# Kernel tuning notes

Hardware: AMD Instinct MI355X
Metric: run time of the kernel (lower is better)

## Reference

```python
import jax, jax.numpy as jnp
import numpy as np

B, L, C = 16, 2048, 256
H, R = 6, 32
HEAD_SCALE = 1.0 / np.sqrt(R)


def setup_inputs() -> dict:
    key = jax.random.key(0)
    k1, k2, k3, k4 = jax.random.split(key, 4)
    feats = jax.random.normal(k1, (B, L + 1, C), dtype=jnp.float32)
    Wq = jax.random.normal(k2, (H * R, C), dtype=jnp.float32) * (1.0 / np.sqrt(C))
    Wk = jax.random.normal(k3, (H * R, C), dtype=jnp.float32) * (1.0 / np.sqrt(C))
    Wd = jax.random.normal(k4, (1, C), dtype=jnp.float32) * (1.0 / np.sqrt(C))
    bd = jnp.zeros((1,), dtype=jnp.float32)
    logit_scale = jnp.ones((), dtype=jnp.float32)
    return {"feats": feats, "Wq": Wq, "Wk": Wk, "Wd": Wd, "bd": bd,
            "logit_scale": logit_scale}


def _fold_vertices(feats):
    # drop leading token, pair-average: [B, L+1, C] -> [B, L//2, C]
    x = feats[:, 1:]
    b, l, c = x.shape
    return x.reshape(b, l // 2, 2, c).mean(axis=2)


def reference(feats, Wq, Wk, Wd, bd, logit_scale):
    x = _fold_vertices(feats)                     # [B, N, C]
    b, n, _ = x.shape
    Q = (x @ Wq.T).reshape(b, n, H, R)            # [B, N, H, R]
    K = (x @ Wk.T).reshape(b, n, H, R)
    # sum over heads of per-head low-rank QK^T == contraction over folded (H*R)
    S = jnp.einsum('bnhr,bmhr->bnm', Q, K) * HEAD_SCALE   # [B, N, N]
    d = (x @ Wd.T + bd).squeeze(-1)               # [B, N]
    idx = jnp.arange(n)
    S = S.at[:, idx, idx].add(d)
    return S * jnp.maximum(logit_scale, 0.01)
```

## Files before the change

kernel.cpp:

```cpp
#include <hip/hip_runtime.h>
#include <stdint.h>


#define HD_SCALE 0.17677669529663687f

typedef __bf16 bf16_t;
typedef bf16_t bf16x8 __attribute__((ext_vector_type(8)));
typedef float f32x4 __attribute__((ext_vector_type(4)));

__device__ __forceinline__ unsigned short f2bf(float f) {
  unsigned int u = __float_as_uint(f);
  return (unsigned short)((u + 0x7fffu + ((u >> 16) & 1u)) >> 16);
}

__device__ __forceinline__ void gload16(const void* g, void* l) {
  __builtin_amdgcn_global_load_lds(
      (const __attribute__((address_space(1))) void*)g,
      (__attribute__((address_space(3))) void*)l, 16, 0, 0);
}

__global__ __launch_bounds__(256) void k_prep(const float* __restrict__ feats,
                                              const float* __restrict__ Wq,
                                              const float* __restrict__ Wk,
                                              const float* __restrict__ Wd,
                                              const float* __restrict__ bd,
                                              unsigned short* __restrict__ xb,
                                              float* __restrict__ dvec,
                                              unsigned short* __restrict__ Wqkb) {
  const int t = threadIdx.x;
  if (blockIdx.x < 384) {
    const int idx = blockIdx.x * 256 + t;
    const float v = (idx < 49152) ? Wq[idx] : Wk[idx - 49152];
    Wqkb[idx] = f2bf(v);
  }
  const int wave = t >> 6, lane = t & 63;
  const int gr = blockIdx.x * 4 + wave;
  const int b = gr >> 10, n = gr & 1023;
  const int c = lane * 4;

  const float* r0 = feats + (size_t)(b * 2049 + 1 + 2 * n) * 256 + c;
  float4 p0 = *(const float4*)r0;
  float4 p1 = *(const float4*)(r0 + 256);
  float4 wv = *(const float4*)(Wd + c);

  float x0 = (p0.x + p1.x) * 0.5f;
  float x1 = (p0.y + p1.y) * 0.5f;
  float x2 = (p0.z + p1.z) * 0.5f;
  float x3 = (p0.w + p1.w) * 0.5f;

  ushort4 xs;
  xs.x = f2bf(x0); xs.y = f2bf(x1); xs.z = f2bf(x2); xs.w = f2bf(x3);
  *(ushort4*)&xb[(size_t)gr * 256 + c] = xs;

  float dot = x0 * wv.x + x1 * wv.y + x2 * wv.z + x3 * wv.w;
#pragma unroll
  for (int o = 32; o > 0; o >>= 1) dot += __shfl_down(dot, o, 64);
  if (lane == 0) dvec[gr] = dot + bd[0];
}

__global__ __launch_bounds__(256) void k_proj(const unsigned short* __restrict__ xb,
                                              const unsigned short* __restrict__ Wqkb,
                                              unsigned short* __restrict__ QK) {
  __shared__ unsigned short As[128 * 64];
  __shared__ unsigned short Bs[128 * 64];
  const int t = threadIdx.x;
  const int w = t >> 6, l = t & 63;
  const int m0 = blockIdx.x * 128;
  const int n0 = blockIdx.y * 128;
  const int wm = w >> 1, wn = w & 1;
  const int quad = l >> 4, lr = l & 15;

  f32x4 acc[4][4] = {};

  for (int kk = 0; kk < 4; ++kk) {
    const int k0 = kk * 64;
    __syncthreads();
#pragma unroll
    for (int i = 0; i < 4; ++i) {
      const int e = i * 256 + t;
      const int row = e >> 3;
      const int kc = (e & 7) ^ (row & 7);
      gload16(xb + (size_t)(m0 + row) * 256 + k0 + kc * 8,
              &As[(i * 256 + (w << 6)) * 8]);
      gload16(Wqkb + (size_t)(n0 + row) * 256 + k0 + kc * 8,
              &Bs[(i * 256 + (w << 6)) * 8]);
    }
    __syncthreads();

#pragma unroll
    for (int s = 0; s < 2; ++s) {
      bf16x8 a[4], bb[4];
#pragma unroll
      for (int i = 0; i < 4; ++i) {
        const int row = wm * 64 + i * 16 + lr;
        const int pos = (s * 4 + quad) ^ (row & 7);
        a[i] = *(const bf16x8*)&As[row * 64 + pos * 8];
      }
#pragma unroll
      for (int j = 0; j < 4; ++j) {
        const int row = wn * 64 + j * 16 + lr;
        const int pos = (s * 4 + quad) ^ (row & 7);
        bb[j] = *(const bf16x8*)&Bs[row * 64 + pos * 8];
      }
#pragma unroll
      for (int i = 0; i < 4; ++i)
#pragma unroll
        for (int j = 0; j < 4; ++j)
          acc[i][j] = __builtin_amdgcn_mfma_f32_16x16x32_bf16(a[i], bb[j],
                                                              acc[i][j], 0, 0, 0);
    }
  }

#pragma unroll
  for (int i = 0; i < 4; ++i)
#pragma unroll
    for (int j = 0; j < 4; ++j)
#pragma unroll
      for (int r = 0; r < 4; ++r) {
        const int row = m0 + wm * 64 + i * 16 + quad * 4 + r;
        const int col = n0 + wn * 64 + j * 16 + lr;
        QK[(size_t)row * 384 + col] = f2bf(acc[i][j][r]);
      }
}

__global__ __launch_bounds__(256) void k_score(const unsigned short* __restrict__ QK,
                                               const float* __restrict__ dvec,
                                               const float* __restrict__ logit_scale,
                                               float* __restrict__ out) {
  __shared__ unsigned short As[128 * 64];
  __shared__ unsigned short Bs[128 * 64];
  const int t = threadIdx.x;
  const int w = t >> 6, l = t & 63;
  const int mt = blockIdx.x, nt = blockIdx.y, b = blockIdx.z;
  const int m0 = mt * 128;
  const int n0 = nt * 128;
  const int wm = w >> 1, wn = w & 1;
  const int quad = l >> 4, lr = l & 15;
  const size_t qbase = (size_t)b * 1024 * 384;

  f32x4 acc[4][4] = {};

  for (int kk = 0; kk < 3; ++kk) {
    const int k0 = kk * 64;
    __syncthreads();
#pragma unroll
    for (int i = 0; i < 4; ++i) {
      const int e = i * 256 + t;
      const int row = e >> 3;
      const int kc = (e & 7) ^ (row & 7);
      gload16(QK + qbase + (size_t)(n0 + row) * 384 + k0 + kc * 8,
              &As[(i * 256 + (w << 6)) * 8]);
      gload16(QK + qbase + (size_t)(m0 + row) * 384 + 192 + k0 + kc * 8,
              &Bs[(i * 256 + (w << 6)) * 8]);
    }
    __syncthreads();

#pragma unroll
    for (int s = 0; s < 2; ++s) {
      bf16x8 a[4], bb[4];
#pragma unroll
      for (int i = 0; i < 4; ++i) {
        const int row = wm * 64 + i * 16 + lr;
        const int pos = (s * 4 + quad) ^ (row & 7);
        a[i] = *(const bf16x8*)&As[row * 64 + pos * 8];
      }
#pragma unroll
      for (int j = 0; j < 4; ++j) {
        const int row = wn * 64 + j * 16 + lr;
        const int pos = (s * 4 + quad) ^ (row & 7);
        bb[j] = *(const bf16x8*)&Bs[row * 64 + pos * 8];
      }
#pragma unroll
      for (int i = 0; i < 4; ++i)
#pragma unroll
        for (int j = 0; j < 4; ++j)
          acc[i][j] = __builtin_amdgcn_mfma_f32_16x16x32_bf16(a[i], bb[j],
                                                              acc[i][j], 0, 0, 0);
    }
  }

  const float ls = fmaxf(logit_scale[0], 0.01f);
  const bool diag_block = (m0 == n0);
#pragma unroll
  for (int i = 0; i < 4; ++i)
#pragma unroll
    for (int j = 0; j < 4; ++j)
#pragma unroll
      for (int r = 0; r < 4; ++r) {
        const int nr = n0 + wm * 64 + i * 16 + quad * 4 + r;
        const int mc = m0 + wn * 64 + j * 16 + lr;
        float v = acc[i][j][r] * HD_SCALE;
        if (diag_block && nr == mc) v += dvec[b * 1024 + nr];
        __builtin_nontemporal_store(v * ls,
            &out[((size_t)b << 20) + (size_t)nr * 1024 + mc]);
      }
}

extern "C" void kernel_launch(void* const* d_in, const int* in_sizes, int n_in,
                              void* d_out, int out_size, void* d_ws, size_t ws_size,
                              hipStream_t stream) {
  const float* feats = (const float*)d_in[0];
  const float* Wq = (const float*)d_in[1];
  const float* Wk = (const float*)d_in[2];
  const float* Wd = (const float*)d_in[3];
  const float* bd = (const float*)d_in[4];
  const float* ls = (const float*)d_in[5];
  float* out = (float*)d_out;

  uint8_t* ws = (uint8_t*)d_ws;
  unsigned short* xb = (unsigned short*)ws;
  unsigned short* QK = (unsigned short*)(ws + (8u << 20));
  float* dvec = (float*)(ws + (20u << 20));
  unsigned short* Wqkb = (unsigned short*)(ws + (20u << 20) + (64u << 10));

  hipLaunchKernelGGL(k_prep, dim3(4096), dim3(256), 0, stream, feats, Wq, Wk, Wd, bd,
                     xb, dvec, Wqkb);
  hipLaunchKernelGGL(k_proj, dim3(128, 3), dim3(256), 0, stream, xb, Wqkb, QK);
  hipLaunchKernelGGL(k_score, dim3(8, 8, 16), dim3(256), 0, stream, QK, dvec, ls, out);
}
```

Before: 127.2 us.

## Load MFMA operands directly from global memory, dropping LDS staging in both GEMMs

Both GEMM kernels stop staging tiles in shared memory with global_load_lds plus barriers. Each wave now loads its bf16x8 MFMA fragments straight from global memory and relies on L1/L2 for reuse. The projection kernel also halves its N tile to 64 and doubles the grid so more blocks run. This removes the LDS traffic and __syncthreads stalls, but each operand is fetched redundantly by several waves and there is no explicit prefetch or double buffering.

```diff
diff --git a/kernel.cpp b/kernel.cpp
--- a/kernel.cpp
+++ b/kernel.cpp
@@ -11,12 +11,6 @@
 __device__ __forceinline__ unsigned short f2bf(float f) {
   unsigned int u = __float_as_uint(f);
   return (unsigned short)((u + 0x7fffu + ((u >> 16) & 1u)) >> 16);
-}
-
-__device__ __forceinline__ void gload16(const void* g, void* l) {
-  __builtin_amdgcn_global_load_lds(
-      (const __attribute__((address_space(1))) void*)g,
-      (__attribute__((address_space(3))) void*)l, 16, 0, 0);
 }
 
 __global__ __launch_bounds__(256) void k_prep(const float* __restrict__ feats,
@@ -61,64 +55,42 @@
 __global__ __launch_bounds__(256) void k_proj(const unsigned short* __restrict__ xb,
                                               const unsigned short* __restrict__ Wqkb,
                                               unsigned short* __restrict__ QK) {
-  __shared__ unsigned short As[128 * 64];
-  __shared__ unsigned short Bs[128 * 64];
   const int t = threadIdx.x;
   const int w = t >> 6, l = t & 63;
   const int m0 = blockIdx.x * 128;
-  const int n0 = blockIdx.y * 128;
+  const int n0 = blockIdx.y * 64;
   const int wm = w >> 1, wn = w & 1;
   const int quad = l >> 4, lr = l & 15;
 
-  f32x4 acc[4][4] = {};
+  const unsigned short* ap = xb + (size_t)(m0 + wm * 64 + lr) * 256 + quad * 8;
+  const unsigned short* bp = Wqkb + (size_t)(n0 + wn * 32 + lr) * 256 + quad * 8;
 
-  for (int kk = 0; kk < 4; ++kk) {
-    const int k0 = kk * 64;
-    __syncthreads();
+  f32x4 acc[4][2] = {};
 #pragma unroll
-    for (int i = 0; i < 4; ++i) {
-      const int e = i * 256 + t;
-      const int row = e >> 3;
-      const int kc = (e & 7) ^ (row & 7);
-      gload16(xb + (size_t)(m0 + row) * 256 + k0 + kc * 8,
-              &As[(i * 256 + (w << 6)) * 8]);
-      gload16(Wqkb + (size_t)(n0 + row) * 256 + k0 + kc * 8,
-              &Bs[(i * 256 + (w << 6)) * 8]);
-    }
-    __syncthreads();
-
+  for (int kk = 0; kk < 8; ++kk) {
+    bf16x8 a[4], bb[2];
 #pragma unroll
-    for (int s = 0; s < 2; ++s) {
-      bf16x8 a[4], bb[4];
+    for (int i = 0; i < 4; ++i)
+      a[i] = *(const bf16x8*)(ap + (size_t)(i * 16) * 256 + kk * 32);
 #pragma unroll
-      for (int i = 0; i < 4; ++i) {
-        const int row = wm * 64 + i * 16 + lr;
-        const int pos = (s * 4 + quad) ^ (row & 7);
-        a[i] = *(const bf16x8*)&As[row * 64 + pos * 8];
-      }
+    for (int j = 0; j < 2; ++j)
+      bb[j] = *(const bf16x8*)(bp + (size_t)(j * 16) * 256 + kk * 32);
 #pragma unroll
-      for (int j = 0; j < 4; ++j) {
-        const int row = wn * 64 + j * 16 + lr;
-        const int pos = (s * 4 + quad) ^ (row & 7);
-        bb[j] = *(const bf16x8*)&Bs[row * 64 + pos * 8];
-      }
+    for (int i = 0; i < 4; ++i)
 #pragma unroll
-      for (int i = 0; i < 4; ++i)
-#pragma unroll
-        for (int j = 0; j < 4; ++j)
-          acc[i][j] = __builtin_amdgcn_mfma_f32_16x16x32_bf16(a[i], bb[j],
-                                                              acc[i][j], 0, 0, 0);
-    }
+      for (int j = 0; j < 2; ++j)
+        acc[i][j] = __builtin_amdgcn_mfma_f32_16x16x32_bf16(a[i], bb[j],
+                                                            acc[i][j], 0, 0, 0);
   }
 
 #pragma unroll
   for (int i = 0; i < 4; ++i)
 #pragma unroll
-    for (int j = 0; j < 4; ++j)
+    for (int j = 0; j < 2; ++j)
 #pragma unroll
       for (int r = 0; r < 4; ++r) {
         const int row = m0 + wm * 64 + i * 16 + quad * 4 + r;
-        const int col = n0 + wn * 64 + j * 16 + lr;
+        const int col = n0 + wn * 32 + j * 16 + lr;
         QK[(size_t)row * 384 + col] = f2bf(acc[i][j][r]);
       }
 }
@@ -127,8 +99,6 @@
                                                const float* __restrict__ dvec,
                                                const float* __restrict__ logit_scale,
                                                float* __restrict__ out) {
-  __shared__ unsigned short As[128 * 64];
-  __shared__ unsigned short Bs[128 * 64];
   const int t = threadIdx.x;
   const int w = t >> 6, l = t & 63;
   const int mt = blockIdx.x, nt = blockIdx.y, b = blockIdx.z;
@@ -138,45 +108,25 @@
   const int quad = l >> 4, lr = l & 15;
   const size_t qbase = (size_t)b * 1024 * 384;
 
+  const unsigned short* qp = QK + qbase + (size_t)(n0 + wm * 64 + lr) * 384 + quad * 8;
+  const unsigned short* kp = QK + qbase + (size_t)(m0 + wn * 64 + lr) * 384 + 192 + quad * 8;
+
   f32x4 acc[4][4] = {};
-
-  for (int kk = 0; kk < 3; ++kk) {
-    const int k0 = kk * 64;
-    __syncthreads();
 #pragma unroll
-    for (int i = 0; i < 4; ++i) {
-      const int e = i * 256 + t;
-      const int row = e >> 3;
-      const int kc = (e & 7) ^ (row & 7);
-      gload16(QK + qbase + (size_t)(n0 + row) * 384 + k0 + kc * 8,
-              &As[(i * 256 + (w << 6)) * 8]);
-      gload16(QK + qbase + (size_t)(m0 + row) * 384 + 192 + k0 + kc * 8,
-              &Bs[(i * 256 + (w << 6)) * 8]);
-    }
-    __syncthreads();
-
+  for (int kk = 0; kk < 6; ++kk) {
+    bf16x8 a[4], bb[4];
 #pragma unroll
-    for (int s = 0; s < 2; ++s) {
-      bf16x8 a[4], bb[4];
+    for (int i = 0; i < 4; ++i)
+      a[i] = *(const bf16x8*)(qp + (size_t)(i * 16) * 384 + kk * 32);
 #pragma unroll
-      for (int i = 0; i < 4; ++i) {
-        const int row = wm * 64 + i * 16 + lr;
-        const int pos = (s * 4 + quad) ^ (row & 7);
-        a[i] = *(const bf16x8*)&As[row * 64 + pos * 8];
-      }
+    for (int j = 0; j < 4; ++j)
+      bb[j] = *(const bf16x8*)(kp + (size_t)(j * 16) * 384 + kk * 32);
 #pragma unroll
-      for (int j = 0; j < 4; ++j) {
-        const int row = wn * 64 + j * 16 + lr;
-        const int pos = (s * 4 + quad) ^ (row & 7);
-        bb[j] = *(const bf16x8*)&Bs[row * 64 + pos * 8];
-      }
+    for (int i = 0; i < 4; ++i)
 #pragma unroll
-      for (int i = 0; i < 4; ++i)
-#pragma unroll
-        for (int j = 0; j < 4; ++j)
-          acc[i][j] = __builtin_amdgcn_mfma_f32_16x16x32_bf16(a[i], bb[j],
-                                                              acc[i][j], 0, 0, 0);
-    }
+      for (int j = 0; j < 4; ++j)
+        acc[i][j] = __builtin_amdgcn_mfma_f32_16x16x32_bf16(a[i], bb[j],
+                                                            acc[i][j], 0, 0, 0);
   }
 
   const float ls = fmaxf(logit_scale[0], 0.01f);
@@ -215,6 +165,6 @@
 
   hipLaunchKernelGGL(k_prep, dim3(4096), dim3(256), 0, stream, feats, Wq, Wk, Wd, bd,
                      xb, dvec, Wqkb);
-  hipLaunchKernelGGL(k_proj, dim3(128, 3), dim3(256), 0, stream, xb, Wqkb, QK);
+  hipLaunchKernelGGL(k_proj, dim3(128, 6), dim3(256), 0, stream, xb, Wqkb, QK);
   hipLaunchKernelGGL(k_score, dim3(8, 8, 16), dim3(256), 0, stream, QK, dvec, ls, out);
 }
```

Result: slower. 148.3 us (+16.6%).

## Stage whole K tile in padded LDS once, read Q fragments directly from global

Applied to the files above, without the earlier changes.

The score kernel now loads the entire 128x192 K tile into LDS in a single pass, using a 25-chunk row stride as padding against bank conflicts, and then synchronises only once instead of three times. The Q operand no longer goes through LDS: each wave reads its MFMA A-fragments straight from global memory through the cache. This removes the per-k-step barriers and half of the LDS traffic, but it relies on global load latency and cache hits for Q and gives up the swizzled LDS layout for the A operand.

```diff
diff --git a/kernel.cpp b/kernel.cpp
--- a/kernel.cpp
+++ b/kernel.cpp
@@ -127,8 +127,7 @@
                                                const float* __restrict__ dvec,
                                                const float* __restrict__ logit_scale,
                                                float* __restrict__ out) {
-  __shared__ unsigned short As[128 * 64];
-  __shared__ unsigned short Bs[128 * 64];
+  __shared__ unsigned short Bs[128 * 25 * 8];
   const int t = threadIdx.x;
   const int w = t >> 6, l = t & 63;
   const int mt = blockIdx.x, nt = blockIdx.y, b = blockIdx.z;
@@ -138,45 +137,41 @@
   const int quad = l >> 4, lr = l & 15;
   const size_t qbase = (size_t)b * 1024 * 384;
 
+#pragma unroll
+  for (int i = 0; i < 13; ++i) {
+    const int chunk = i * 256 + t;
+    if (chunk < 3200) {
+      const int row = (int)(((unsigned long long)chunk * 1374389535ull) >> 35);
+      int pos = chunk - row * 25;
+      if (pos > 23) pos = 23;
+      gload16(QK + qbase + (size_t)(m0 + row) * 384 + 192 + pos * 8,
+              &Bs[(size_t)(i * 256 + (w << 6)) * 8]);
+    }
+  }
+
+  const unsigned short* qp =
+      QK + qbase + (size_t)(n0 + wm * 64 + lr) * 384 + quad * 8;
+
+  __syncthreads();
+
   f32x4 acc[4][4] = {};
-
-  for (int kk = 0; kk < 3; ++kk) {
-    const int k0 = kk * 64;
-    __syncthreads();
-#pragma unroll
-    for (int i = 0; i < 4; ++i) {
-      const int e = i * 256 + t;
-      const int row = e >> 3;
-      const int kc = (e & 7) ^ (row & 7);
-      gload16(QK + qbase + (size_t)(n0 + row) * 384 + k0 + kc * 8,
-              &As[(i * 256 + (w << 6)) * 8]);
-      gload16(QK + qbase + (size_t)(m0 + row) * 384 + 192 + k0 + kc * 8,
-              &Bs[(i * 256 + (w << 6)) * 8]);
-    }
-    __syncthreads();
-
-#pragma unroll
-    for (int s = 0; s < 2; ++s) {
-      bf16x8 a[4], bb[4];
-#pragma unroll
-      for (int i = 0; i < 4; ++i) {
-        const int row = wm * 64 + i * 16 + lr;
-        const int pos = (s * 4 + quad) ^ (row & 7);
-        a[i] = *(const bf16x8*)&As[row * 64 + pos * 8];
-      }
-#pragma unroll
-      for (int j = 0; j < 4; ++j) {
-        const int row = wn * 64 + j * 16 + lr;
-        const int pos = (s * 4 + quad) ^ (row & 7);
-        bb[j] = *(const bf16x8*)&Bs[row * 64 + pos * 8];
-      }
-#pragma unroll
-      for (int i = 0; i < 4; ++i)
-#pragma unroll
-        for (int j = 0; j < 4; ++j)
-          acc[i][j] = __builtin_amdgcn_mfma_f32_16x16x32_bf16(a[i], bb[j],
-                                                              acc[i][j], 0, 0, 0);
-    }
+#pragma unroll
+  for (int kk = 0; kk < 6; ++kk) {
+    bf16x8 a[4], bb[4];
+#pragma unroll
+    for (int i = 0; i < 4; ++i)
+      a[i] = *(const bf16x8*)(qp + (size_t)(i * 16) * 384 + kk * 32);
+#pragma unroll
+    for (int j = 0; j < 4; ++j) {
+      const int row = wn * 64 + j * 16 + lr;
+      bb[j] = *(const bf16x8*)&Bs[(row * 25 + kk * 4 + quad) * 8];
+    }
+#pragma unroll
+    for (int i = 0; i < 4; ++i)
+#pragma unroll
+      for (int j = 0; j < 4; ++j)
+        acc[i][j] = __builtin_amdgcn_mfma_f32_16x16x32_bf16(a[i], bb[j],
+                                                            acc[i][j], 0, 0, 0);
   }
 
   const float ls = fmaxf(logit_scale[0], 0.01f);
```

Measured after the change: 133.3 us. +4.8%, slower.
